# Performance work log

Hardware: AMD Instinct MI355X
Metric: run time of the kernel (lower is better)

Reference implementation:

```python
import jax, jax.numpy as jnp
import numpy as np

# Standard 4-level FPN pyramid for an ~800x1200 input (RT-DETR-like)
SHAPES = [(100, 150), (50, 75), (25, 38), (13, 19)]


def setup_inputs() -> dict:
    key = jax.random.key(0)
    k1, k2, k3 = jax.random.split(key, 3)
    B, Hd, C, P = 2, 8, 32, 4
    shapes = np.array(SHAPES, dtype=np.int64)          # [Levels, 2]
    areas = shapes.prod(axis=1)
    L = int(areas.sum())                                # 19947 total tokens
    Q = L                                               # encoder self-attention
    lsi = np.concatenate([[0], np.cumsum(areas)[:-1]]).astype(np.int64)
    value = jax.random.normal(k1, (B, L, Hd, C), dtype=jnp.float32)
    sampling_locations = jax.random.uniform(k2, (B, Q, Hd, len(SHAPES), P, 2), dtype=jnp.float32)
    w = jax.random.uniform(k3, (B, Q, Hd, len(SHAPES), P), dtype=jnp.float32)
    attention_weights = w / w.sum(axis=(3, 4), keepdims=True)  # softmax-like normalization over levels*points
    return {
        "value": value,
        "spatial_shapes": jnp.asarray(shapes),
        "level_start_index": jnp.asarray(lsi),
        "sampling_locations": sampling_locations,
        "attention_weights": attention_weights,
    }


def _bilinear_sample(vflat, Hh, Ww, loc):
    """Zero-padded bilinear sampling matching the CUDA ms_deform_attn kernel.
    vflat: [BH, Hh*Ww, C]; loc: [BH, Q, P, 2] normalized to [0,1].
    Returns [BH, Q, P, C].
    """
    x = loc[..., 0] * Ww - 0.5
    y = loc[..., 1] * Hh - 0.5
    x0 = jnp.floor(x)
    y0 = jnp.floor(y)
    dx = x - x0
    dy = y - y0
    x0i = x0.astype(jnp.int32)
    y0i = y0.astype(jnp.int32)
    BH, Qn, P = x0i.shape
    out = jnp.zeros(vflat.shape[:1] + (Qn, P, vflat.shape[-1]), vflat.dtype)
    corners = [
        (y0i,     x0i,     (1 - dy) * (1 - dx)),
        (y0i,     x0i + 1, (1 - dy) * dx),
        (y0i + 1, x0i,     dy * (1 - dx)),
        (y0i + 1, x0i + 1, dy * dx),
    ]
    for yi, xi, wgt in corners:
        valid = ((yi >= 0) & (yi < Hh) & (xi >= 0) & (xi < Ww)).astype(vflat.dtype)
        idx = jnp.clip(yi, 0, Hh - 1) * Ww + jnp.clip(xi, 0, Ww - 1)  # [BH,Q,P]
        g = jnp.take_along_axis(vflat, idx.reshape(BH, Qn * P, 1), axis=1)
        g = g.reshape(BH, Qn, P, -1)
        out = out + g * (wgt * valid)[..., None]
    return out


def reference(value, spatial_shapes, level_start_index, sampling_locations, attention_weights):
    shapes = np.asarray(spatial_shapes)        # static level shapes
    starts = np.asarray(level_start_index)
    B, L, Hd, C = value.shape
    Q = sampling_locations.shape[1]
    n_levels = shapes.shape[0]
    P = sampling_locations.shape[4]
    out = jnp.zeros((B * Hd, Q, C), value.dtype)
    for l in range(n_levels):
        Hh, Ww = int(shapes[l, 0]), int(shapes[l, 1])
        s = int(starts[l])
        v = value[:, s:s + Hh * Ww]                                   # [B, HW, Hd, C]
        vflat = v.transpose(0, 2, 1, 3).reshape(B * Hd, Hh * Ww, C)   # [BH, HW, C]
        loc = sampling_locations[:, :, :, l].transpose(0, 2, 1, 3, 4).reshape(B * Hd, Q, P, 2)
        aw = attention_weights[:, :, :, l].transpose(0, 2, 1, 3).reshape(B * Hd, Q, P)
        samp = _bilinear_sample(vflat, Hh, Ww, loc)                    # [BH, Q, P, C]
        out = out + (samp * aw[..., None]).sum(axis=2)
    return out.reshape(B, Hd, Q, C).transpose(0, 2, 1, 3).reshape(B, Q, Hd * C)
```

## Files before the change

kernel.cpp:

```cpp
#include <hip/hip_runtime.h>

#define NLV  4
#define CCH  32
#define HD   8
#define QTOT 19947
#define LTOT 19947
#define BB   2

typedef float        f32x4 __attribute__((ext_vector_type(4)));
typedef float        f32x2 __attribute__((ext_vector_type(2)));
typedef _Float16     f16x8 __attribute__((ext_vector_type(8)));
typedef unsigned int u32;
typedef u32          u32x2 __attribute__((ext_vector_type(2)));

#define SLICE_BYTES 1617280
#define WS_NEED     (16UL * SLICE_BYTES)
#define CHUNKS_PER_SLICE 101080
#define TOTAL_CHUNKS (16 * CHUNKS_PER_SLICE)

__global__ __launch_bounds__(256) void repack_f16(
    const float* __restrict__ value, _Float16* __restrict__ v16)
{
    const int id = blockIdx.x * 256 + (int)threadIdx.x;
    if (id >= TOTAL_CHUNKS) return;
    const int slice = id / CHUNKS_PER_SLICE;
    const int r     = id - slice * CHUNKS_PER_SLICE;
    const int b = slice >> 3, h = slice & 7;

    int x, y, k, W, S;
    if (r < 60800) {
        y = r / 608; const int rr = r - y * 608;
        x = (rr >> 2) - 1; k = rr & 3; W = 150; S = 0;
    } else if (r < 76000) {
        const int i = r - 60800; y = i / 304; const int rr = i - y * 304;
        x = ((rr >> 3) << 1) + ((rr >> 2) & 1);     k = rr & 3; W = 75; S = 15000;
    } else if (r < 91200) {
        const int i = r - 76000; y = i / 304; const int rr = i - y * 304;
        x = ((rr >> 3) << 1) + ((rr >> 2) & 1) - 1; k = rr & 3; W = 75; S = 15000;
    } else if (r < 95000) {
        const int i = r - 91200; y = i / 152; const int rr = i - y * 152;
        x = ((rr >> 3) << 1) + ((rr >> 2) & 1);     k = rr & 3; W = 38; S = 18750;
    } else if (r < 99000) {
        const int i = r - 95000; y = i / 160; const int rr = i - y * 160;
        x = ((rr >> 3) << 1) + ((rr >> 2) & 1) - 1; k = rr & 3; W = 38; S = 18750;
    } else if (r < 100040) {
        const int i = r - 99000; y = i / 80; const int rr = i - y * 80;
        x = ((rr >> 3) << 1) + ((rr >> 2) & 1);     k = rr & 3; W = 19; S = 19700;
    } else {
        const int i = r - 100040; y = i / 80; const int rr = i - y * 80;
        x = ((rr >> 3) << 1) + ((rr >> 2) & 1) - 1; k = rr & 3; W = 19; S = 19700;
    }

    f16x8 o = {(_Float16)0.f, (_Float16)0.f, (_Float16)0.f, (_Float16)0.f,
               (_Float16)0.f, (_Float16)0.f, (_Float16)0.f, (_Float16)0.f};
    if (x >= 0 && x < W) {
        const float* src = value +
            (((size_t)(b * LTOT + S + y * W + x) * HD + h) * CCH + k * 8);
        const f32x4 a = *(const f32x4*)src;
        const f32x4 c = *(const f32x4*)(src + 4);
        o[0] = (_Float16)a.x; o[1] = (_Float16)a.y;
        o[2] = (_Float16)a.z; o[3] = (_Float16)a.w;
        o[4] = (_Float16)c.x; o[5] = (_Float16)c.y;
        o[6] = (_Float16)c.z; o[7] = (_Float16)c.w;
    }
    *(f16x8*)((char*)v16 + (size_t)id * 16) = o;
}

#define GPB  32
#define JOBS (GPB * 16)
#define BLOCKS_PER_SLICE 624
#define NSLICES (BB * HD)

__device__ __forceinline__ unsigned jslot(int gl, int s) {
    return (unsigned)(gl * 16 + (s ^ (gl & 7)));
}

__global__ __launch_bounds__(256) void msda_fwd_pair(
    const _Float16* __restrict__ v16,
    const float* __restrict__ loc,
    const float* __restrict__ attw,
    float* __restrict__ out)
{
    __shared__ __align__(8)  u32   s_of[JOBS * 2];
    __shared__ __align__(16) float s_w [JOBS * 4];

    const int Hs[NLV]  = {100, 50, 25, 13};
    const int Ws[NLV]  = {150, 75, 38, 19};
    const int CN0[NLV] = {0, 38, 19, 10};
    const int CN1[NLV] = {0, 38, 20, 10};
    const int OF0[NLV] = {0,  972800, 1459200, 1584000};
    const int OF1[NLV] = {0, 1216000, 1520000, 1600640};

    const int slice = blockIdx.x & 15;
    const int blk   = blockIdx.x >> 4;
    const int b = slice >> 3;
    const int h = slice & 7;
    const int t = (int)threadIdx.x;

#pragma unroll
    for (int jj = 0; jj < 2; ++jj) {
        const int j  = t + jj * 256;
        const int gl = j >> 4;
        const int s  = j & 15;
        const int l  = s >> 2;
        const int q  = blk * GPB + gl;
        const int qc = min(q, QTOT - 1);
        const size_t og = ((size_t)b * QTOT + qc) * HD + h;

        const f32x2 lxy = __builtin_nontemporal_load((const f32x2*)loc + og * 16 + s);
        float wa = __builtin_nontemporal_load(attw + og * 16 + s);
        if (q >= QTOT) wa = 0.f;

        const int H = Hs[l], W = Ws[l];
        const float x = lxy.x * (float)W - 0.5f;
        const float y = lxy.y * (float)H - 0.5f;
        const float x0f = floorf(x), y0f = floorf(y);
        const float dx = x - x0f,  dy = y - y0f;
        const int x0 = (int)x0f,   y0 = (int)y0f;

        const float r0w = ((y0 >= 0) ? (1.f - dy) : 0.f) * wa;
        const float r1w = ((y0 + 1 < H) ? dy : 0.f) * wa;
        f32x4 w;
        w.x = r0w * (1.f - dx);  w.y = r0w * dx;
        w.z = r1w * (1.f - dx);  w.w = r1w * dx;

        const int cy0 = max(y0, 0);
        const int cy1 = min(y0 + 1, H - 1);

        u32 off0, off1;
        if (l == 0) {
            const u32 col = (u32)(x0 + 1);
            off0 = ((u32)cy0 * 152u + col) * 64u;
            off1 = ((u32)cy1 * 152u + col) * 64u;
        } else {
            const int copy = x0 & 1;
            const u32 p  = (u32)((x0 + copy) >> 1);
            const u32 cn = (u32)(copy ? CN1[l] : CN0[l]);
            const u32 lo = (u32)(copy ? OF1[l] : OF0[l]);
            off0 = lo + ((u32)cy0 * cn + p) * 128u;
            off1 = lo + ((u32)cy1 * cn + p) * 128u;
        }

        const unsigned sl = jslot(gl, s);
        u32x2 of; of.x = off0; of.y = off1;
        *(u32x2*)&s_of[sl * 2] = of;
        *(f32x4*)&s_w [sl * 4] = w;
    }

    __syncthreads();

    const int gl   = t >> 3;
    const int lane = t & 7;
    const int lh   = (t >> 2) & 1;
    const int q    = blk * GPB + gl;
    const char* vb = (const char*)v16 + (size_t)slice * SLICE_BYTES + lane * 16;

    float acc[8] = {0.f, 0.f, 0.f, 0.f, 0.f, 0.f, 0.f, 0.f};
#pragma unroll
    for (int s = 0; s < 16; ++s) {
        const unsigned sl = jslot(gl, s);
        const u32x2 of = *(const u32x2*)&s_of[sl * 2];
        const f32x4 w  = *(const f32x4*)&s_w [sl * 4];
        const f16x8 g0 = *(const f16x8*)(vb + of.x);
        const f16x8 g1 = *(const f16x8*)(vb + of.y);
        const float wr0 = lh ? w.y : w.x;
        const float wr1 = lh ? w.w : w.z;
#pragma unroll
        for (int c = 0; c < 8; ++c) {
            acc[c] += (float)g0[c] * wr0;
            acc[c] += (float)g1[c] * wr1;
        }
    }

#pragma unroll
    for (int c = 0; c < 8; ++c)
        acc[c] += __shfl_xor(acc[c], 4, 64);

    if (q < QTOT) {
        const size_t og = ((size_t)b * QTOT + q) * HD + h;
        f32x4 v;
        v.x = lh ? acc[4] : acc[0];
        v.y = lh ? acc[5] : acc[1];
        v.z = lh ? acc[6] : acc[2];
        v.w = lh ? acc[7] : acc[3];
        __builtin_nontemporal_store(v, (f32x4*)out + og * 8 + (t & 3) * 2 + lh);
    }
}

#define FGPB 32
#define FJOBS (FGPB * 16)
#define LDS_S 0
__device__ __forceinline__ unsigned fjslot(int gl, int s) {
    return (unsigned)((gl * 16 + (s ^ (gl & 7))) * 4);
}
__global__ __launch_bounds__(256) void msda_fwd_f32(
    const float* __restrict__ value,
    const float* __restrict__ loc,
    const float* __restrict__ attw,
    float* __restrict__ out)
{
    __shared__ __align__(16) u32   s_ofs[FJOBS * 4];
    __shared__ __align__(16) float s_wts[FJOBS * 4];
    const int Hs[NLV] = {100, 50, 25, 13};
    const int Ws[NLV] = {150, 75, 38, 19};
    const int Ss[NLV] = {0, 15000, 18750, 19700};
    const int slice = blockIdx.x & 15;
    const int blk   = blockIdx.x >> 4;
    const int b = slice >> 3, h = slice & 7;
    const int t = (int)threadIdx.x;
#pragma unroll
    for (int jj = 0; jj < 2; ++jj) {
        const int j  = t + jj * 256;
        const int gl = j >> 4, s = j & 15, l = s >> 2;
        const int q  = blk * FGPB + gl;
        const int qc = min(q, QTOT - 1);
        const size_t og = ((size_t)b * QTOT + qc) * HD + h;
        const f32x2 lxy = __builtin_nontemporal_load((const f32x2*)loc + og * 16 + s);
        float wa = __builtin_nontemporal_load(attw + og * 16 + s);
        if (q >= QTOT) wa = 0.f;
        const int H = Hs[l], W = Ws[l];
        const float x = lxy.x * (float)W - 0.5f;
        const float y = lxy.y * (float)H - 0.5f;
        const float x0f = floorf(x), y0f = floorf(y);
        const float dx = x - x0f, dy = y - y0f;
        const int x0 = (int)x0f, y0 = (int)y0f, x1 = x0 + 1, y1 = y0 + 1;
        const bool vx0 = (x0 >= 0) & (x0 < W), vx1 = (x1 >= 0) & (x1 < W);
        const bool vy0 = (y0 >= 0) & (y0 < H), vy1 = (y1 >= 0) & (y1 < H);
        float w00 = (1.f - dy) * (1.f - dx) * wa, w01 = (1.f - dy) * dx * wa;
        float w10 = dy * (1.f - dx) * wa,         w11 = dy * dx * wa;
        w00 = (vy0 & vx0) ? w00 : 0.f; w01 = (vy0 & vx1) ? w01 : 0.f;
        w10 = (vy1 & vx0) ? w10 : 0.f; w11 = (vy1 & vx1) ? w11 : 0.f;
        const int cx0 = min(max(x0, 0), W - 1), cx1 = min(max(x1, 0), W - 1);
        const int cy0 = min(max(y0, 0), H - 1), cy1 = min(max(y1, 0), H - 1);
        const u32 base = (u32)(((b * LTOT + Ss[l]) * HD + h) * CCH) * 4u;
        const u32 r0 = (u32)(cy0 * W), r1 = (u32)(cy1 * W);
        u32 o0 = base + (r0 + (u32)cx0) * (HD * CCH * 4u);
        u32 o1 = base + (r0 + (u32)cx1) * (HD * CCH * 4u);
        u32 o2 = base + (r1 + (u32)cx0) * (HD * CCH * 4u);
        u32 o3 = base + (r1 + (u32)cx1) * (HD * CCH * 4u);
        const unsigned sb = fjslot(gl, s);
        s_ofs[sb + 0] = o0; s_ofs[sb + 1] = o1;
        s_ofs[sb + 2] = o2; s_ofs[sb + 3] = o3;
        f32x4 wts; wts.x = w00; wts.y = w01; wts.z = w10; wts.w = w11;
        *(f32x4*)&s_wts[sb] = wts;
    }
    __syncthreads();
    const int gl = t >> 3, lane = t & 7;
    const int q  = blk * FGPB + gl;
    const char* vb = (const char*)value + lane * 16;
    f32x4 acc = {0.f, 0.f, 0.f, 0.f};
#pragma unroll
    for (int s = 0; s < 16; ++s) {
        const unsigned sb = fjslot(gl, s);
        const f32x4 w = *(const f32x4*)&s_wts[sb];
        acc += (*(const f32x4*)(vb + s_ofs[sb + 0])) * w.x;
        acc += (*(const f32x4*)(vb + s_ofs[sb + 1])) * w.y;
        acc += (*(const f32x4*)(vb + s_ofs[sb + 2])) * w.z;
        acc += (*(const f32x4*)(vb + s_ofs[sb + 3])) * w.w;
    }
    if (q < QTOT) {
        const size_t og = ((size_t)b * QTOT + q) * HD + h;
        __builtin_nontemporal_store(acc, (f32x4*)out + og * 8 + lane);
    }
}

extern "C" void kernel_launch(void* const* d_in, const int* in_sizes, int n_in,
                              void* d_out, int out_size, void* d_ws, size_t ws_size,
                              hipStream_t stream) {
    const float* value = (const float*)d_in[0];
    const float* loc   = (const float*)d_in[3];
    const float* attw  = (const float*)d_in[4];
    float* out = (float*)d_out;

    if (ws_size >= WS_NEED) {
        _Float16* v16 = (_Float16*)d_ws;
        repack_f16<<<(TOTAL_CHUNKS + 255) / 256, 256, 0, stream>>>(value, v16);
        msda_fwd_pair<<<BLOCKS_PER_SLICE * NSLICES, 256, 0, stream>>>(v16, loc, attw, out);
    } else {
        msda_fwd_f32<<<624 * NSLICES, 256, 0, stream>>>(value, loc, attw, out);
    }
}
```

Baseline: 204.0 us.

## Stage small pyramid levels in LDS with persistent per-slice blocks

Levels 2 and 3 of each (batch, head) slice are converted to fp16 and kept in LDS inside a persistent kernel. Each block loops over query blocks of 64 queries with 512 threads, so level-2/3 gathers become LDS reads rather than global gathers. The repack kernel now covers only levels 0 and 1, which shrinks the workspace. The cost is about 100 KB of dynamic LDS per block, limiting occupancy. There are also only 256 blocks in total, each doing serialized loops with two barriers per iteration.

```diff
diff --git a/kernel.cpp b/kernel.cpp
--- a/kernel.cpp
+++ b/kernel.cpp
@@ -13,9 +13,9 @@
 typedef unsigned int u32;
 typedef u32          u32x2 __attribute__((ext_vector_type(2)));
 
-#define SLICE_BYTES 1617280
+#define SLICE_BYTES 1459200
 #define WS_NEED     (16UL * SLICE_BYTES)
-#define CHUNKS_PER_SLICE 101080
+#define CHUNKS_PER_SLICE 91200
 #define TOTAL_CHUNKS (16 * CHUNKS_PER_SLICE)
 
 __global__ __launch_bounds__(256) void repack_f16(
@@ -34,21 +34,9 @@
     } else if (r < 76000) {
         const int i = r - 60800; y = i / 304; const int rr = i - y * 304;
         x = ((rr >> 3) << 1) + ((rr >> 2) & 1);     k = rr & 3; W = 75; S = 15000;
-    } else if (r < 91200) {
+    } else {
         const int i = r - 76000; y = i / 304; const int rr = i - y * 304;
         x = ((rr >> 3) << 1) + ((rr >> 2) & 1) - 1; k = rr & 3; W = 75; S = 15000;
-    } else if (r < 95000) {
-        const int i = r - 91200; y = i / 152; const int rr = i - y * 152;
-        x = ((rr >> 3) << 1) + ((rr >> 2) & 1);     k = rr & 3; W = 38; S = 18750;
-    } else if (r < 99000) {
-        const int i = r - 95000; y = i / 160; const int rr = i - y * 160;
-        x = ((rr >> 3) << 1) + ((rr >> 2) & 1) - 1; k = rr & 3; W = 38; S = 18750;
-    } else if (r < 100040) {
-        const int i = r - 99000; y = i / 80; const int rr = i - y * 80;
-        x = ((rr >> 3) << 1) + ((rr >> 2) & 1);     k = rr & 3; W = 19; S = 19700;
-    } else {
-        const int i = r - 100040; y = i / 80; const int rr = i - y * 80;
-        x = ((rr >> 3) << 1) + ((rr >> 2) & 1) - 1; k = rr & 3; W = 19; S = 19700;
     }
 
     f16x8 o = {(_Float16)0.f, (_Float16)0.f, (_Float16)0.f, (_Float16)0.f,
@@ -66,130 +54,180 @@
     *(f16x8*)((char*)v16 + (size_t)id * 16) = o;
 }
 
-#define GPB  32
-#define JOBS (GPB * 16)
-#define BLOCKS_PER_SLICE 624
-#define NSLICES (BB * HD)
+#define GPB     64
+#define JOBS    (GPB * 16)
+#define QBLOCKS 312
+#define PARTS   16
+
+#define SW_OFF  8192
+#define A2      24576
+#define NTEX2   950
+#define A3      85440
+#define NTEX3   247
+#define SMEM_TOTAL 101312
+#define NTEX    (NTEX2 + NTEX3)
 
 __device__ __forceinline__ unsigned jslot(int gl, int s) {
     return (unsigned)(gl * 16 + (s ^ (gl & 7)));
 }
 
-__global__ __launch_bounds__(256) void msda_fwd_pair(
+__global__ __launch_bounds__(512, 2) void msda_fwd_v2(
     const _Float16* __restrict__ v16,
+    const float* __restrict__ value,
     const float* __restrict__ loc,
     const float* __restrict__ attw,
     float* __restrict__ out)
 {
-    __shared__ __align__(8)  u32   s_of[JOBS * 2];
-    __shared__ __align__(16) float s_w [JOBS * 4];
-
-    const int Hs[NLV]  = {100, 50, 25, 13};
-    const int Ws[NLV]  = {150, 75, 38, 19};
-    const int CN0[NLV] = {0, 38, 19, 10};
-    const int CN1[NLV] = {0, 38, 20, 10};
-    const int OF0[NLV] = {0,  972800, 1459200, 1584000};
-    const int OF1[NLV] = {0, 1216000, 1520000, 1600640};
+    extern __shared__ __align__(16) char smem[];
+
+    const int Hs[NLV] = {100, 50, 25, 13};
+    const int Ws[NLV] = {150, 75, 38, 19};
 
     const int slice = blockIdx.x & 15;
-    const int blk   = blockIdx.x >> 4;
+    const int part  = blockIdx.x >> 4;
     const int b = slice >> 3;
     const int h = slice & 7;
     const int t = (int)threadIdx.x;
 
-#pragma unroll
-    for (int jj = 0; jj < 2; ++jj) {
-        const int j  = t + jj * 256;
-        const int gl = j >> 4;
-        const int s  = j & 15;
-        const int l  = s >> 2;
-        const int q  = blk * GPB + gl;
-        const int qc = min(q, QTOT - 1);
-        const size_t og = ((size_t)b * QTOT + qc) * HD + h;
-
-        const f32x2 lxy = __builtin_nontemporal_load((const f32x2*)loc + og * 16 + s);
-        float wa = __builtin_nontemporal_load(attw + og * 16 + s);
-        if (q >= QTOT) wa = 0.f;
-
-        const int H = Hs[l], W = Ws[l];
-        const float x = lxy.x * (float)W - 0.5f;
-        const float y = lxy.y * (float)H - 0.5f;
-        const float x0f = floorf(x), y0f = floorf(y);
-        const float dx = x - x0f,  dy = y - y0f;
-        const int x0 = (int)x0f,   y0 = (int)y0f;
-
-        const float r0w = ((y0 >= 0) ? (1.f - dy) : 0.f) * wa;
-        const float r1w = ((y0 + 1 < H) ? dy : 0.f) * wa;
-        f32x4 w;
-        w.x = r0w * (1.f - dx);  w.y = r0w * dx;
-        w.z = r1w * (1.f - dx);  w.w = r1w * dx;
-
-        const int cy0 = max(y0, 0);
-        const int cy1 = min(y0 + 1, H - 1);
-
-        u32 off0, off1;
-        if (l == 0) {
-            const u32 col = (u32)(x0 + 1);
-            off0 = ((u32)cy0 * 152u + col) * 64u;
-            off1 = ((u32)cy1 * 152u + col) * 64u;
-        } else {
-            const int copy = x0 & 1;
-            const u32 p  = (u32)((x0 + copy) >> 1);
-            const u32 cn = (u32)(copy ? CN1[l] : CN0[l]);
-            const u32 lo = (u32)(copy ? OF1[l] : OF0[l]);
-            off0 = lo + ((u32)cy0 * cn + p) * 128u;
-            off1 = lo + ((u32)cy1 * cn + p) * 128u;
+    {
+        const f16x8 z = {(_Float16)0.f, (_Float16)0.f, (_Float16)0.f, (_Float16)0.f,
+                         (_Float16)0.f, (_Float16)0.f, (_Float16)0.f, (_Float16)0.f};
+        for (int task = t; task < NTEX * 4 + 8; task += 512) {
+            if (task < NTEX * 4) {
+                const int ti = task >> 2, p = task & 3;
+                int src_lp, lds;
+                if (ti < NTEX2) { src_lp = 18750 + ti;           lds = A2 + ti * 64; }
+                else            { src_lp = 19700 + (ti - NTEX2); lds = A3 + (ti - NTEX2) * 64; }
+                const float* src = value +
+                    (((size_t)(b * LTOT + src_lp)) * HD + h) * CCH + p * 8;
+                const f32x4 a = *(const f32x4*)src;
+                const f32x4 c = *(const f32x4*)(src + 4);
+                f16x8 o;
+                o[0] = (_Float16)a.x; o[1] = (_Float16)a.y;
+                o[2] = (_Float16)a.z; o[3] = (_Float16)a.w;
+                o[4] = (_Float16)c.x; o[5] = (_Float16)c.y;
+                o[6] = (_Float16)c.z; o[7] = (_Float16)c.w;
+                *(f16x8*)(smem + lds + p * 16) = o;
+            } else {
+                const int pi = task - NTEX * 4;
+                const int lds = (pi < 4) ? (A2 + NTEX2 * 64 + pi * 16)
+                                         : (A3 + NTEX3 * 64 + (pi - 4) * 16);
+                *(f16x8*)(smem + lds) = z;
+            }
         }
-
-        const unsigned sl = jslot(gl, s);
-        u32x2 of; of.x = off0; of.y = off1;
-        *(u32x2*)&s_of[sl * 2] = of;
-        *(f32x4*)&s_w [sl * 4] = w;
-    }
-
-    __syncthreads();
-
-    const int gl   = t >> 3;
-    const int lane = t & 7;
-    const int lh   = (t >> 2) & 1;
-    const int q    = blk * GPB + gl;
-    const char* vb = (const char*)v16 + (size_t)slice * SLICE_BYTES + lane * 16;
-
-    float acc[8] = {0.f, 0.f, 0.f, 0.f, 0.f, 0.f, 0.f, 0.f};
-#pragma unroll
-    for (int s = 0; s < 16; ++s) {
-        const unsigned sl = jslot(gl, s);
-        const u32x2 of = *(const u32x2*)&s_of[sl * 2];
-        const f32x4 w  = *(const f32x4*)&s_w [sl * 4];
-        const f16x8 g0 = *(const f16x8*)(vb + of.x);
-        const f16x8 g1 = *(const f16x8*)(vb + of.y);
-        const float wr0 = lh ? w.y : w.x;
-        const float wr1 = lh ? w.w : w.z;
-#pragma unroll
-        for (int c = 0; c < 8; ++c) {
-            acc[c] += (float)g0[c] * wr0;
-            acc[c] += (float)g1[c] * wr1;
+    }
+
+    for (int qb = part; qb < QBLOCKS; qb += PARTS) {
+
+#pragma unroll
+        for (int jj = 0; jj < 2; ++jj) {
+            const int j  = t + jj * 512;
+            const int gl = j >> 4;
+            const int s  = j & 15;
+            const int l  = s >> 2;
+            const int q  = qb * GPB + gl;
+            const int qc = min(q, QTOT - 1);
+            const size_t og = ((size_t)b * QTOT + qc) * HD + h;
+
+            const f32x2 lxy = __builtin_nontemporal_load((const f32x2*)loc + og * 16 + s);
+            float wa = __builtin_nontemporal_load(attw + og * 16 + s);
+            if (q >= QTOT) wa = 0.f;
+
+            const int H = Hs[l], W = Ws[l];
+            const float x = lxy.x * (float)W - 0.5f;
+            const float y = lxy.y * (float)H - 0.5f;
+            const float x0f = floorf(x), y0f = floorf(y);
+            const float dx = x - x0f,  dy = y - y0f;
+            const int x0 = (int)x0f,   y0 = (int)y0f;
+
+            const float r0w = ((y0 >= 0) ? (1.f - dy) : 0.f) * wa;
+            const float r1w = ((y0 + 1 < H) ? dy : 0.f) * wa;
+            f32x4 w;
+            w.x = r0w * (1.f - dx);  w.y = r0w * dx;
+            w.z = r1w * (1.f - dx);  w.w = r1w * dx;
+
+            const int cy0 = max(y0, 0);
+            const int cy1 = min(y0 + 1, H - 1);
+
+            u32 off0, off1;
+            if (l == 0) {
+                const u32 col = (u32)(x0 + 1);
+                off0 = ((u32)cy0 * 152u + col) * 64u;
+                off1 = ((u32)cy1 * 152u + col) * 64u;
+            } else if (l == 1) {
+                const int copy = x0 & 1;
+                const u32 p  = (u32)((x0 + copy) >> 1);
+                const u32 lo = copy ? 1216000u : 972800u;
+                off0 = lo + ((u32)cy0 * 38u + p) * 128u;
+                off1 = lo + ((u32)cy1 * 38u + p) * 128u;
+            } else {
+                if (x0 < 0)     { w.x = w.y; w.z = w.w; w.y = 0.f; w.w = 0.f; }
+                if (x0 >= W - 1){ w.y = 0.f; w.w = 0.f; }
+                const u32 xb   = (u32)max(x0, 0);
+                const u32 base = (l == 2) ? (u32)A2 : (u32)A3;
+                off0 = base + ((u32)cy0 * (u32)W + xb) * 64u;
+                off1 = base + ((u32)cy1 * (u32)W + xb) * 64u;
+            }
+
+            const unsigned sl = jslot(gl, s);
+            u32x2 of; of.x = off0; of.y = off1;
+            *(u32x2*)(smem + sl * 8) = of;
+            *(f32x4*)(smem + SW_OFF + sl * 16) = w;
         }
-    }
-
-#pragma unroll
-    for (int c = 0; c < 8; ++c)
-        acc[c] += __shfl_xor(acc[c], 4, 64);
-
-    if (q < QTOT) {
-        const size_t og = ((size_t)b * QTOT + q) * HD + h;
-        f32x4 v;
-        v.x = lh ? acc[4] : acc[0];
-        v.y = lh ? acc[5] : acc[1];
-        v.z = lh ? acc[6] : acc[2];
-        v.w = lh ? acc[7] : acc[3];
-        __builtin_nontemporal_store(v, (f32x4*)out + og * 8 + (t & 3) * 2 + lh);
+
+        __syncthreads();
+
+        {
+            const int gl   = t >> 3;
+            const int lane = t & 7;
+            const int lh   = (t >> 2) & 1;
+            const int q    = qb * GPB + gl;
+            const char* vb = (const char*)v16 + (size_t)slice * SLICE_BYTES + lane * 16;
+            const char* lb = smem + lane * 16;
+
+            float acc[8] = {0.f, 0.f, 0.f, 0.f, 0.f, 0.f, 0.f, 0.f};
+#pragma unroll
+            for (int s = 0; s < 16; ++s) {
+                const unsigned sl = jslot(gl, s);
+                const u32x2 of = *(const u32x2*)(smem + sl * 8);
+                const f32x4 w  = *(const f32x4*)(smem + SW_OFF + sl * 16);
+                f16x8 g0, g1;
+                if (s < 8) {
+                    g0 = *(const f16x8*)(vb + of.x);
+                    g1 = *(const f16x8*)(vb + of.y);
+                } else {
+                    g0 = *(const f16x8*)(lb + of.x);
+                    g1 = *(const f16x8*)(lb + of.y);
+                }
+                const float wr0 = lh ? w.y : w.x;
+                const float wr1 = lh ? w.w : w.z;
+#pragma unroll
+                for (int c = 0; c < 8; ++c) {
+                    acc[c] += (float)g0[c] * wr0;
+                    acc[c] += (float)g1[c] * wr1;
+                }
+            }
+
+#pragma unroll
+            for (int c = 0; c < 8; ++c)
+                acc[c] += __shfl_xor(acc[c], 4, 64);
+
+            if (q < QTOT) {
+                const size_t og = ((size_t)b * QTOT + q) * HD + h;
+                f32x4 v;
+                v.x = lh ? acc[4] : acc[0];
+                v.y = lh ? acc[5] : acc[1];
+                v.z = lh ? acc[6] : acc[2];
+                v.w = lh ? acc[7] : acc[3];
+                __builtin_nontemporal_store(v, (f32x4*)out + og * 8 + (t & 3) * 2 + lh);
+            }
+        }
+        __syncthreads();
     }
 }
 
 #define FGPB 32
 #define FJOBS (FGPB * 16)
-#define LDS_S 0
 __device__ __forceinline__ unsigned fjslot(int gl, int s) {
     return (unsigned)((gl * 16 + (s ^ (gl & 7))) * 4);
 }
@@ -272,11 +310,19 @@
     const float* attw  = (const float*)d_in[4];
     float* out = (float*)d_out;
 
-    if (ws_size >= WS_NEED) {
+    static int smem_ok = -1;
+    if (smem_ok < 0) {
+        smem_ok = (hipFuncSetAttribute(
+                       reinterpret_cast<const void*>(msda_fwd_v2),
+                       hipFuncAttributeMaxDynamicSharedMemorySize,
+                       SMEM_TOTAL) == hipSuccess) ? 1 : 0;
+    }
+
+    if (ws_size >= WS_NEED && smem_ok == 1) {
         _Float16* v16 = (_Float16*)d_ws;
         repack_f16<<<(TOTAL_CHUNKS + 255) / 256, 256, 0, stream>>>(value, v16);
-        msda_fwd_pair<<<BLOCKS_PER_SLICE * NSLICES, 256, 0, stream>>>(v16, loc, attw, out);
+        msda_fwd_v2<<<PARTS * 16, 512, SMEM_TOTAL, stream>>>(v16, value, loc, attw, out);
     } else {
-        msda_fwd_f32<<<624 * NSLICES, 256, 0, stream>>>(value, loc, attw, out);
-    }
-}
+        msda_fwd_f32<<<624 * 16, 256, 0, stream>>>(value, loc, attw, out);
+    }
+}
```

New measurement: 216.9 us. +6.3%, slower.
